# Optimization experiments

Hardware: AMD Instinct MI355X
Metric: run time of the kernel (lower is better)

The kernel has to match this reference:

```python
import jax, jax.numpy as jnp
import numpy as np

DIM = 1024

def setup_inputs() -> dict:
    key = jax.random.key(0)
    k1, k2, k3, k4, k5 = jax.random.split(key, 5)
    B, Sq, Skv = 8, 2048, 2048
    x = jax.random.normal(k1, (B, Sq, DIM), dtype=jnp.float32)
    context = jax.random.normal(k2, (B, Skv, DIM), dtype=jnp.float32)
    # nn.Linear default init scale ~ uniform; use scaled normal for stability
    s = DIM ** -0.5
    Wq = jax.random.normal(k3, (DIM, DIM), dtype=jnp.float32) * s
    Wk = jax.random.normal(k4, (DIM, DIM), dtype=jnp.float32) * s
    Wv = jax.random.normal(k5, (DIM, DIM), dtype=jnp.float32) * s
    return {"x": x, "context": context, "Wq": Wq, "Wk": Wk, "Wv": Wv}

def reference(x, context, Wq, Wk, Wv):
    # Linear with weight W applied as x @ W.T (torch convention); here W is [out, in]
    q = jnp.einsum('bsd,ed->bse', x, Wq)          # [B, Sq, D]
    k = jnp.einsum('btd,ed->bte', context, Wk)    # [B, Skv, D]
    v = jnp.einsum('btd,ed->bte', context, Wv)    # [B, Skv, D]
    scale = Wq.shape[0] ** -0.5                   # dim ** -0.5 (no head split)
    dots = jnp.einsum('bse,bte->bst', q, k) * scale  # [B, Sq, Skv]
    attn = jax.nn.softmax(dots, axis=-1)
    out = jnp.einsum('bst,bte->bse', attn, v)     # [B, Sq, D]
    return out
```

## Files before the change

kernel.cpp:

```cpp
#include <hip/hip_runtime.h>


typedef unsigned short u16;
typedef __bf16 bf16x8 __attribute__((ext_vector_type(8)));
typedef float f32x4 __attribute__((ext_vector_type(4)));
typedef u16 us8 __attribute__((ext_vector_type(8)));

__device__ __forceinline__ u16 f2bf(float f) {
  unsigned int u = __float_as_uint(f);
  u += 0x7fffu + ((u >> 16) & 1u);
  return (u16)(u >> 16);
}
__device__ __forceinline__ float bf2f(u16 h) {
  return __uint_as_float((unsigned int)h << 16);
}

struct __attribute__((aligned(8))) us4 { u16 x, y, z, w; };

__global__ __launch_bounds__(256) void cvt_xc(const float4* __restrict__ x,
                                              const float4* __restrict__ c,
                                              us4* __restrict__ dx,
                                              us4* __restrict__ dc) {
  int i = blockIdx.x * 256 + threadIdx.x;
  const float4* s = (i < 4194304) ? x : (c - 4194304);
  us4* d = (i < 4194304) ? dx : (dc - 4194304);
  float4 v = s[i];
  us4 o{f2bf(v.x), f2bf(v.y), f2bf(v.z), f2bf(v.w)};
  d[i] = o;
}

__global__ __launch_bounds__(256) void cvt_w(const float4* __restrict__ wq,
                                             const float4* __restrict__ wk,
                                             const float4* __restrict__ wv,
                                             us4* __restrict__ d) {
  int i = blockIdx.x * 256 + threadIdx.x;
  const float4* s; float sc;
  if (i < 262144)      { s = wq;           sc = 0.03125f; }
  else if (i < 524288) { s = wk - 262144;  sc = 1.0f; }
  else                 { s = wv - 524288;  sc = 1.0f; }
  float4 v = s[i];
  us4 o{f2bf(v.x * sc), f2bf(v.y * sc), f2bf(v.z * sc), f2bf(v.w * sc)};
  d[i] = o;
}

__device__ __forceinline__ void gload16(const u16* g, u16* l) {
  __builtin_amdgcn_global_load_lds(
      (const __attribute__((address_space(1))) unsigned int*)g,
      (__attribute__((address_space(3))) unsigned int*)l,
      16, 0, 0);
}

template <bool BF16OUT>
__global__ __launch_bounds__(512, 2) void gemm_nt(
    const u16* __restrict__ A, const u16* __restrict__ B, void* __restrict__ Cout,
    int lda, int ldb, int ldc, int K,
    long batchA, long batchB, long batchC, int nx, int ny) {
  __shared__ u16 lds[65536];

  const int p    = blockIdx.x;
  const int slab = gridDim.x >> 3;
  const int gid  = (p & 7) * slab + (p >> 3);
  const int bx   = gid % nx;
  const int t2   = gid / nx;
  const int by   = t2 % ny;
  const int z    = t2 / ny;

  const int tid  = threadIdx.x;
  const int lane = tid & 63;
  const int wv   = tid >> 6;

  const u16* Ab = A + (size_t)z * batchA + (size_t)by * 256 * lda;
  const u16* Bb = B + (size_t)z * batchB + (size_t)bx * 256 * ldb;

  const int srow = tid >> 2;
  const int scol = ((tid & 3) ^ ((tid >> 3) & 3)) * 8;

  const u16* gA = Ab + (size_t)srow * lda + scol;
  const u16* gB = Bb + (size_t)srow * ldb + scol;
  const size_t a128 = (size_t)128 * lda, b128 = (size_t)128 * ldb;

  u16* dA = &lds[tid * 8];
  u16* dB = &lds[16384 + tid * 8];

  const int fr = lane & 15;
  const int xw = (((lane >> 4) ^ ((lane >> 1) & 3)) * 8);
  const int wm = (wv >> 2) * 128;
  const int wn = (wv & 3) * 64;
  const int rA = (wm + fr) * 32 + xw;
  const int rB = (wn + fr) * 32 + xw;

  const unsigned ldsb = (unsigned)(size_t)&lds[0];
  const unsigned bA0 = ldsb + (unsigned)(rA * 2);
  const unsigned bB0 = ldsb + 32768u + (unsigned)(rB * 2);

  f32x4 acc[8][4];
#pragma unroll
  for (int i = 0; i < 8; i++)
#pragma unroll
    for (int j = 0; j < 4; j++) acc[i][j] = (f32x4)0.f;

  const int NTt = K >> 6;

#define STAGE_A(BUF, KT, H) do {                                  \
    const u16* g_ = gA + (size_t)(KT) * 64 + (H) * 32;            \
    u16* d_ = dA + ((BUF) << 15) + (H) * 8192;                    \
    gload16(g_, d_); gload16(g_ + a128, d_ + 4096); } while (0)
#define STAGE_B(BUF, KT, H) do {                                  \
    const u16* g_ = gB + (size_t)(KT) * 64 + (H) * 32;            \
    u16* d_ = dB + ((BUF) << 15) + (H) * 8192;                    \
    gload16(g_, d_); gload16(g_ + b128, d_ + 4096); } while (0)
#define DSR(D, BASE, IMM)                                         \
    asm volatile("ds_read_b128 %0, %1 offset:" #IMM               \
                 : "=v"(D) : "v"(BASE))
#define LGKM0 do { asm volatile("s_waitcnt lgkmcnt(0)" ::: "memory"); \
    __builtin_amdgcn_sched_barrier(0); } while (0)
#define MFMA16(AR)                                                \
    __builtin_amdgcn_s_setprio(1);                                \
    _Pragma("unroll")                                             \
    for (int mi_ = 0; mi_ < 4; mi_++)                             \
      _Pragma("unroll")                                           \
      for (int ni_ = 0; ni_ < 4; ni_++)                           \
        acc[(AR) + mi_][ni_] = __builtin_amdgcn_mfma_f32_16x16x32_bf16( \
            __builtin_bit_cast(bf16x8, av[mi_]),                  \
            __builtin_bit_cast(bf16x8, bv[ni_]),                  \
            acc[(AR) + mi_][ni_], 0, 0, 0);                       \
    __builtin_amdgcn_s_setprio(0);

  STAGE_A(0, 0, 0); STAGE_B(0, 0, 0); STAGE_A(0, 0, 1); STAGE_B(0, 0, 1);
  asm volatile("s_waitcnt vmcnt(4)" ::: "memory");
  __builtin_amdgcn_s_barrier();

  for (int kt = 0; kt < NTt; ++kt) {
    const unsigned bufo = (kt & 1) ? 65536u : 0u;
    const unsigned bA = bA0 + bufo;
    const unsigned bB = bB0 + bufo;
    const int nb = (kt & 1) ^ 1;
    const bool pf = (kt + 1 < NTt);
    f32x4 av[4], bv[4];

    DSR(av[0], bA, 0);     DSR(av[1], bA, 1024);
    DSR(av[2], bA, 2048);  DSR(av[3], bA, 3072);
    DSR(bv[0], bB, 0);     DSR(bv[1], bB, 1024);
    DSR(bv[2], bB, 2048);  DSR(bv[3], bB, 3072);
    if (pf) STAGE_A(nb, kt + 1, 0);
    __builtin_amdgcn_s_barrier();
    LGKM0;
    MFMA16(0)
    __builtin_amdgcn_s_barrier();

    DSR(av[0], bA, 4096);  DSR(av[1], bA, 5120);
    DSR(av[2], bA, 6144);  DSR(av[3], bA, 7168);
    if (pf) STAGE_B(nb, kt + 1, 0);
    __builtin_amdgcn_s_barrier();
    LGKM0;
    MFMA16(4)
    if (pf) { asm volatile("s_waitcnt vmcnt(4)" ::: "memory"); }
    else    { asm volatile("s_waitcnt vmcnt(0)" ::: "memory"); }
    __builtin_amdgcn_s_barrier();

    DSR(av[0], bA, 16384); DSR(av[1], bA, 17408);
    DSR(av[2], bA, 18432); DSR(av[3], bA, 19456);
    DSR(bv[0], bB, 16384); DSR(bv[1], bB, 17408);
    DSR(bv[2], bB, 18432); DSR(bv[3], bB, 19456);
    if (pf) STAGE_A(nb, kt + 1, 1);
    __builtin_amdgcn_s_barrier();
    LGKM0;
    MFMA16(0)
    __builtin_amdgcn_s_barrier();

    DSR(av[0], bA, 20480); DSR(av[1], bA, 21504);
    DSR(av[2], bA, 22528); DSR(av[3], bA, 23552);
    if (pf) STAGE_B(nb, kt + 1, 1);
    __builtin_amdgcn_s_barrier();
    LGKM0;
    MFMA16(4)
    if (pf) {
      asm volatile("s_waitcnt vmcnt(4)" ::: "memory");
      __builtin_amdgcn_s_barrier();
    }
  }

  const size_t cbase = (size_t)z * batchC;
  const int row0 = by * 256 + wm + (lane >> 4) * 4;
  const int col0 = bx * 256 + wn + fr;
#pragma unroll
  for (int mi = 0; mi < 8; mi++) {
#pragma unroll
    for (int i = 0; i < 4; i++) {
      const size_t roff = cbase + (size_t)(row0 + mi * 16 + i) * ldc + col0;
#pragma unroll
      for (int ni = 0; ni < 4; ni++) {
        float v = acc[mi][ni][i];
        if constexpr (BF16OUT)
          ((u16*)Cout)[roff + ni * 16] = f2bf(v);
        else
          ((float*)Cout)[roff + ni * 16] = v;
      }
    }
  }
#undef STAGE_A
#undef STAGE_B
#undef DSR
#undef LGKM0
#undef MFMA16
}

__global__ __launch_bounds__(256) void softmax_rows_bf16(u16* __restrict__ SP) {
  const size_t row = blockIdx.x;
  us8* p = (us8*)(SP + row * 2048);
  const int t = threadIdx.x;
  us8 raw = p[t];
  float v[8];
#pragma unroll
  for (int i = 0; i < 8; i++) v[i] = bf2f(raw[i]);

  float m = v[0];
#pragma unroll
  for (int i = 1; i < 8; i++) m = fmaxf(m, v[i]);
#pragma unroll
  for (int o = 32; o; o >>= 1) m = fmaxf(m, __shfl_xor(m, o, 64));
  __shared__ float redm[4];
  if ((t & 63) == 0) redm[t >> 6] = m;
  __syncthreads();
  m = fmaxf(fmaxf(redm[0], redm[1]), fmaxf(redm[2], redm[3]));

  float sum = 0.f;
#pragma unroll
  for (int i = 0; i < 8; i++) { v[i] = __expf(v[i] - m); sum += v[i]; }
#pragma unroll
  for (int o = 32; o; o >>= 1) sum += __shfl_xor(sum, o, 64);
  __shared__ float reds[4];
  if ((t & 63) == 0) reds[t >> 6] = sum;
  __syncthreads();
  sum = reds[0] + reds[1] + reds[2] + reds[3];
  const float r = 1.0f / sum;

  us8 o;
#pragma unroll
  for (int i = 0; i < 8; i++) o[i] = f2bf(v[i] * r);
  p[t] = o;
}

extern "C" void kernel_launch(void* const* d_in, const int* in_sizes, int n_in,
                              void* d_out, int out_size, void* d_ws, size_t ws_size,
                              hipStream_t stream) {
  const float* x   = (const float*)d_in[0];
  const float* ctx = (const float*)d_in[1];
  const float* Wq  = (const float*)d_in[2];
  const float* Wk  = (const float*)d_in[3];
  const float* Wv  = (const float*)d_in[4];
  float* out = (float*)d_out;

  const size_t NT = 8ull * 2048 * 1024;

  u16* wsu  = (u16*)d_ws;
  u16* xbf  = wsu;
  u16* cbf  = wsu + NT;
  u16* Sbuf = wsu;
  u16* Vt   = wsu + 2 * NT;
  u16* Wqb  = wsu + 3 * NT;
  u16* Qbf = (u16*)d_out;

  dim3 blk(256), gblk(512);

  cvt_xc<<<dim3(32768), blk, 0, stream>>>((const float4*)x, (const float4*)ctx,
                                          (us4*)xbf, (us4*)cbf);
  cvt_w<<<dim3(3072), blk, 0, stream>>>((const float4*)Wq, (const float4*)Wk,
                                        (const float4*)Wv, (us4*)Wqb);

  gemm_nt<true><<<dim3(512), gblk, 0, stream>>>(
      xbf, Wqb, Qbf, 1024, 1024, 1024, 1024,
      (long)NT, 1024L * 1024, (long)NT, 4, 64);
  gemm_nt<true><<<dim3(256), gblk, 0, stream>>>(
      Wqb + 2 * 1024 * 1024, cbf, Vt, 1024, 1024, 2048, 1024,
      0L, 2048L * 1024, 1024L * 2048, 8, 4);

  gemm_nt<true><<<dim3(512), gblk, 0, stream>>>(
      Qbf, Qbf + NT, Sbuf, 1024, 1024, 2048, 1024,
      2048L * 1024, 2048L * 1024, 2048L * 2048, 8, 8);

  softmax_rows_bf16<<<dim3(16384), blk, 0, stream>>>(Sbuf);

  gemm_nt<false><<<dim3(256), gblk, 0, stream>>>(
      Sbuf, Vt, out, 2048, 2048, 1024, 2048,
      2048L * 2048, 1024L * 2048, 2048L * 1024, 4, 8);
}
```

Before: 438.7 us.

## Restructure GEMM k-loop to drop intra-iteration barriers and pipeline LDS reads

The GEMM main loop now issues all four next-tile global-to-LDS prefetches at the start of each iteration. It also loads the LDS fragments into separate register sets (a0/a1/b0/c0/c1/d0), so ds_reads for the next MFMA block overlap the current MFMAs, gated by partial lgkmcnt waits. This removes the barriers between the four sub-phases and keeps a single vmcnt(0) plus barrier at the end of the iteration. The goal is less synchronisation stall and better overlap of LDS reads with MFMA. In exchange it holds more fragment registers, which may cost occupancy, and waits for the whole global prefetch at once.

```diff
diff --git a/kernel.cpp b/kernel.cpp
--- a/kernel.cpp
+++ b/kernel.cpp
@@ -112,23 +112,25 @@
 #define DSR(D, BASE, IMM)                                         \
     asm volatile("ds_read_b128 %0, %1 offset:" #IMM               \
                  : "=v"(D) : "v"(BASE))
-#define LGKM0 do { asm volatile("s_waitcnt lgkmcnt(0)" ::: "memory"); \
+#define LGKM(N) do {                                              \
+    asm volatile("s_waitcnt lgkmcnt(" #N ")" ::: "memory");       \
     __builtin_amdgcn_sched_barrier(0); } while (0)
-#define MFMA16(AR)                                                \
+#define MFMA16(AR, AV, BV)                                        \
     __builtin_amdgcn_s_setprio(1);                                \
     _Pragma("unroll")                                             \
     for (int mi_ = 0; mi_ < 4; mi_++)                             \
       _Pragma("unroll")                                           \
       for (int ni_ = 0; ni_ < 4; ni_++)                           \
         acc[(AR) + mi_][ni_] = __builtin_amdgcn_mfma_f32_16x16x32_bf16( \
-            __builtin_bit_cast(bf16x8, av[mi_]),                  \
-            __builtin_bit_cast(bf16x8, bv[ni_]),                  \
+            __builtin_bit_cast(bf16x8, AV[mi_]),                  \
+            __builtin_bit_cast(bf16x8, BV[ni_]),                  \
             acc[(AR) + mi_][ni_], 0, 0, 0);                       \
     __builtin_amdgcn_s_setprio(0);
 
   STAGE_A(0, 0, 0); STAGE_B(0, 0, 0); STAGE_A(0, 0, 1); STAGE_B(0, 0, 1);
-  asm volatile("s_waitcnt vmcnt(4)" ::: "memory");
+  asm volatile("s_waitcnt vmcnt(0)" ::: "memory");
   __builtin_amdgcn_s_barrier();
+  __builtin_amdgcn_sched_barrier(0);
 
   for (int kt = 0; kt < NTt; ++kt) {
     const unsigned bufo = (kt & 1) ? 65536u : 0u;
@@ -136,47 +138,38 @@
     const unsigned bB = bB0 + bufo;
     const int nb = (kt & 1) ^ 1;
     const bool pf = (kt + 1 < NTt);
-    f32x4 av[4], bv[4];
-
-    DSR(av[0], bA, 0);     DSR(av[1], bA, 1024);
-    DSR(av[2], bA, 2048);  DSR(av[3], bA, 3072);
-    DSR(bv[0], bB, 0);     DSR(bv[1], bB, 1024);
-    DSR(bv[2], bB, 2048);  DSR(bv[3], bB, 3072);
-    if (pf) STAGE_A(nb, kt + 1, 0);
-    __builtin_amdgcn_s_barrier();
-    LGKM0;
-    MFMA16(0)
-    __builtin_amdgcn_s_barrier();
-
-    DSR(av[0], bA, 4096);  DSR(av[1], bA, 5120);
-    DSR(av[2], bA, 6144);  DSR(av[3], bA, 7168);
-    if (pf) STAGE_B(nb, kt + 1, 0);
-    __builtin_amdgcn_s_barrier();
-    LGKM0;
-    MFMA16(4)
-    if (pf) { asm volatile("s_waitcnt vmcnt(4)" ::: "memory"); }
-    else    { asm volatile("s_waitcnt vmcnt(0)" ::: "memory"); }
-    __builtin_amdgcn_s_barrier();
-
-    DSR(av[0], bA, 16384); DSR(av[1], bA, 17408);
-    DSR(av[2], bA, 18432); DSR(av[3], bA, 19456);
-    DSR(bv[0], bB, 16384); DSR(bv[1], bB, 17408);
-    DSR(bv[2], bB, 18432); DSR(bv[3], bB, 19456);
-    if (pf) STAGE_A(nb, kt + 1, 1);
-    __builtin_amdgcn_s_barrier();
-    LGKM0;
-    MFMA16(0)
-    __builtin_amdgcn_s_barrier();
-
-    DSR(av[0], bA, 20480); DSR(av[1], bA, 21504);
-    DSR(av[2], bA, 22528); DSR(av[3], bA, 23552);
-    if (pf) STAGE_B(nb, kt + 1, 1);
-    __builtin_amdgcn_s_barrier();
-    LGKM0;
-    MFMA16(4)
+    f32x4 a0[4], a1[4], b0[4], c0[4], c1[4], d0[4];
+
+    DSR(a0[0], bA, 0);     DSR(a0[1], bA, 1024);
+    DSR(a0[2], bA, 2048);  DSR(a0[3], bA, 3072);
+    DSR(b0[0], bB, 0);     DSR(b0[1], bB, 1024);
+    DSR(b0[2], bB, 2048);  DSR(b0[3], bB, 3072);
+    DSR(a1[0], bA, 4096);  DSR(a1[1], bA, 5120);
+    DSR(a1[2], bA, 6144);  DSR(a1[3], bA, 7168);
+    if (pf) { STAGE_A(nb, kt + 1, 0); STAGE_B(nb, kt + 1, 0);
+              STAGE_A(nb, kt + 1, 1); STAGE_B(nb, kt + 1, 1); }
+
+    LGKM(4);
+    MFMA16(0, a0, b0)
+
+    DSR(c0[0], bA, 16384); DSR(c0[1], bA, 17408);
+    DSR(c0[2], bA, 18432); DSR(c0[3], bA, 19456);
+    DSR(d0[0], bB, 16384); DSR(d0[1], bB, 17408);
+    DSR(d0[2], bB, 18432); DSR(d0[3], bB, 19456);
+    LGKM(8);
+    MFMA16(4, a1, b0)
+
+    DSR(c1[0], bA, 20480); DSR(c1[1], bA, 21504);
+    DSR(c1[2], bA, 22528); DSR(c1[3], bA, 23552);
+    LGKM(4);
+    MFMA16(0, c0, d0)
+    LGKM(0);
+    MFMA16(4, c1, d0)
+
     if (pf) {
-      asm volatile("s_waitcnt vmcnt(4)" ::: "memory");
+      asm volatile("s_waitcnt vmcnt(0)" ::: "memory");
       __builtin_amdgcn_s_barrier();
+      __builtin_amdgcn_sched_barrier(0);
     }
   }
 
@@ -201,7 +194,7 @@
 #undef STAGE_A
 #undef STAGE_B
 #undef DSR
-#undef LGKM0
+#undef LGKM
 #undef MFMA16
 }
 
```

Result: faster. 429.1 us (-2.2%).
